# Performance work log

Measured on AMD Instinct MI355X. Metric: run time of the kernel, lower is better.

The kernel has to match this reference:

```python
import jax, jax.numpy as jnp
import numpy as np

IN_F = 128
OUT_F = 64
HEAD = 4
ALPHA = 0.1
N, S = 32, 1024
OH = OUT_F * HEAD


def setup_inputs() -> dict:
    key = jax.random.key(0)
    k_h, k_adj, k_W, k_a = jax.random.split(key, 4)
    h = jax.random.normal(k_h, (N, S, IN_F), dtype=jnp.float32)
    adj = jax.random.uniform(k_adj, (N, S, S), dtype=jnp.float32)
    # xavier_uniform with gain=1.414
    gain = 1.414
    lim_W = gain * np.sqrt(6.0 / (IN_F + OH))
    W = jax.random.uniform(k_W, (IN_F, OH), dtype=jnp.float32, minval=-lim_W, maxval=lim_W)
    lim_a = gain * np.sqrt(6.0 / (2 * OH + 1))
    a = jax.random.uniform(k_a, (2 * OH, 1), dtype=jnp.float32, minval=-lim_a, maxval=lim_a)
    return {"h": h, "adj": adj, "W": W, "a": a}


def reference(h, adj, W, a):
    # h: (N, S, F_in); adj unused in original forward
    Wh = jnp.einsum('nsf,fo->nso', h, W)  # (N, S, OH)
    a1 = a[:OH, 0]   # source half of concat weight
    a2 = a[OH:, 0]   # target half
    # concat([Wh_i, Wh_j]) @ a == Wh_i@a1 + Wh_j@a2  (avoids (N,S,S,2*OH) tensor)
    f = Wh @ a1  # (N, S)
    g = Wh @ a2  # (N, S)
    e = f[:, :, None] + g[:, None, :]          # (N, S, S)
    e = jnp.where(e > 0, e, ALPHA * e)          # LeakyReLU
    attention = jax.nn.softmax(e, axis=2)
    out = jnp.einsum('nij,njo->nio', attention, Wh)  # (N, S, OH)
    # split into HEAD chunks of OUT_F, stack, mean over heads
    out = out.reshape(N, S, HEAD, OUT_F).mean(axis=2)
    # ELU
    return jnp.where(out > 0, out, jnp.expm1(out))
```

## Files before the change

kernel.cpp:

```cpp
#include <hip/hip_runtime.h>
#include <math.h>

#define NB   32
#define SQ   1024
#define INF  128
#define OUTF 64
#define OHH  256

using bf16x8 = __attribute__((ext_vector_type(8))) __bf16;
using bf16x4 = __attribute__((ext_vector_type(4))) __bf16;
using f32x4  = __attribute__((ext_vector_type(4))) float;

__global__ __launch_bounds__(256) void kA(
    const float* __restrict__ h, const float* __restrict__ W,
    const float* __restrict__ a, __bf16* __restrict__ whmH,
    __bf16* __restrict__ whmL, float* __restrict__ fo, float* __restrict__ go)
{
    __shared__ float WMl[INF][68];
    __shared__ float hT[INF][68];
    __shared__ float al[2 * OHH];
    __shared__ float fgp[8][64];

    const int t  = threadIdx.x;
    const int R0 = blockIdx.x * 64;

    al[t]       = a[t];
    al[t + 256] = a[t + 256];

    for (int idx = t; idx < INF * OUTF; idx += 256) {
        int k = idx >> 6, c = idx & 63;
        const float* Wr = W + k * OHH + c;
        WMl[k][c] = 0.25f * (Wr[0] + Wr[64] + Wr[128] + Wr[192]);
    }

    {
        const int r  = t >> 2;
        const int kq = (t & 3) << 2;
        const float* hrow = h + (size_t)(R0 + r) * INF;
        #pragma unroll
        for (int it = 0; it < 8; ++it) {
            int k0 = it * 16 + kq;
            float4 v = *(const float4*)(hrow + k0);
            hT[k0 + 0][r] = v.x; hT[k0 + 1][r] = v.y;
            hT[k0 + 2][r] = v.z; hT[k0 + 3][r] = v.w;
        }
    }
    __syncthreads();

    if (t < INF) {
        const float4* Wr = (const float4*)(W + t * OHH);
        const float4* a1 = (const float4*)al;
        const float4* a2 = (const float4*)(al + OHH);
        float sf = 0.f, sg = 0.f;
        for (int q = 0; q < OHH / 4; ++q) {
            float4 wv = Wr[q], x1 = a1[q], x2 = a2[q];
            sf += wv.x * x1.x + wv.y * x1.y + wv.z * x1.z + wv.w * x1.w;
            sg += wv.x * x2.x + wv.y * x2.y + wv.z * x2.z + wv.w * x2.w;
        }
        WMl[t][64] = sf;
        WMl[t][65] = sg;
    }
    __syncthreads();

    const int tx = t & 15, ty = t >> 4;
    const int c0 = tx << 2, r0 = ty << 2;
    float acc[4][4] = {};
    #pragma unroll 4
    for (int k = 0; k < INF; ++k) {
        f32x4 av = *(const f32x4*)&hT[k][r0];
        f32x4 bv = *(const f32x4*)&WMl[k][c0];
        #pragma unroll
        for (int i = 0; i < 4; ++i)
            #pragma unroll
            for (int j = 0; j < 4; ++j)
                acc[i][j] += av[i] * bv[j];
    }

    {
        const int n    = R0 >> 10;
        const int J    = ((R0 & 1023) >> 5) + (ty >> 3);
        const int quad = (ty & 7) >> 1;
        const int idx0 = (ty & 1) << 2;
        const int T    = tx >> 2;
        #pragma unroll
        for (int jj = 0; jj < 4; ++jj) {
            const int cl   = ((tx & 3) << 2) + jj;
            const int lane = quad * 16 + cl;
            const size_t base =
                (((size_t)(n * 32 + J) * 4 + T) * 64 + lane) * 8 + idx0;
            bf16x4 hv, lv;
            #pragma unroll
            for (int i = 0; i < 4; ++i) {
                float p  = acc[i][jj];
                __bf16 hb = (__bf16)p;
                hv[i] = hb;
                lv[i] = (__bf16)(p - (float)hb);
            }
            *(bf16x4*)(whmH + base) = hv;
            *(bf16x4*)(whmL + base) = lv;
        }
    }

    {
        const int r = t & 63, grp = t >> 6;
        float sf = 0.f, sg = 0.f;
        for (int k = grp * 32; k < grp * 32 + 32; ++k) {
            float hv = hT[k][r];
            sf += hv * WMl[k][64];
            sg += hv * WMl[k][65];
        }
        fgp[grp][r]     = sf;
        fgp[4 + grp][r] = sg;
    }
    __syncthreads();
    if (t < 64) {
        fo[R0 + t] = fgp[0][t] + fgp[1][t] + fgp[2][t] + fgp[3][t];
    } else if (t < 128) {
        int r = t - 64;
        go[R0 + r] = fgp[4][r] + fgp[5][r] + fgp[6][r] + fgp[7][r];
    }
}

__global__ __launch_bounds__(256) void kC(
    const __bf16* __restrict__ whmH, const __bf16* __restrict__ whmL,
    const float* __restrict__ fi, const float* __restrict__ gi,
    float* __restrict__ out)
{
    __shared__ float  gl[SQ];
    __shared__ float  fl[64];
    __shared__ __bf16 bfr[3][4096];

    const int t     = threadIdx.x;
    const int lane  = t & 63;
    const int wid   = t >> 6;
    const int n     = blockIdx.x & 31;
    const int itile = blockIdx.x >> 5;
    const int i0    = itile * 64;

    const char* gHb = (const char*)(whmH + (size_t)n * 65536) + wid * 1024 + lane * 16;
    const char* gLb = (const char*)(whmL + (size_t)n * 65536) + wid * 1024 + lane * 16;

    auto stage = [&](int J, int buf) {
        char* lH = (char*)&bfr[buf][0] + wid * 1024;
        char* lL = (char*)&bfr[buf][2048] + wid * 1024;
        __builtin_amdgcn_global_load_lds(
            (const __attribute__((address_space(1))) unsigned int*)(gHb + (size_t)J * 4096),
            (__attribute__((address_space(3))) unsigned int*)lH, 16, 0, 0);
        __builtin_amdgcn_global_load_lds(
            (const __attribute__((address_space(1))) unsigned int*)(gLb + (size_t)J * 4096),
            (__attribute__((address_space(3))) unsigned int*)lL, 16, 0, 0);
    };

    ((float4*)gl)[t] = ((const float4*)(gi + n * SQ))[t];
    if (t < 64) fl[t] = fi[n * SQ + i0 + t];

    stage(0, 0);
    stage(1, 1);
    __syncthreads();

    const float myf = fl[wid * 16 + (lane & 15)];
    const int   kq  = lane >> 4;

    f32x4 acc[4] = {};
    float lsum = 0.f;

    for (int J = 0; J < 32; ++J) {
        float p[8];
        {
            const float4 g0 = *(const float4*)&gl[J * 32 + kq * 8];
            const float4 g1 = *(const float4*)&gl[J * 32 + kq * 8 + 4];
            float gs8[8] = {g0.x, g0.y, g0.z, g0.w, g1.x, g1.y, g1.z, g1.w};
            #pragma unroll
            for (int idx = 0; idx < 8; ++idx) {
                float e  = myf + gs8[idx];
                float lr = 0.55f * e + 0.45f * fabsf(e);
                p[idx] = __expf(lr);
            }
        }
        lsum += ((p[0] + p[1]) + (p[2] + p[3])) + ((p[4] + p[5]) + (p[6] + p[7]));

        bf16x8 ph, pl;
        #pragma unroll
        for (int idx = 0; idx < 8; ++idx) {
            __bf16 hb = (__bf16)p[idx];
            ph[idx] = hb;
            pl[idx] = (__bf16)(p[idx] - (float)hb);
        }

        __syncthreads();
        if (J + 2 < 32) stage(J + 2, (J + 2) % 3);

        const bf16x8* fr = (const bf16x8*)&bfr[J % 3][0];
        #pragma unroll
        for (int T = 0; T < 4; ++T) {
            bf16x8 bh = fr[T * 64 + lane];
            bf16x8 bl = fr[(4 + T) * 64 + lane];
            acc[T] = __builtin_amdgcn_mfma_f32_16x16x32_bf16(ph, bh, acc[T], 0, 0, 0);
            acc[T] = __builtin_amdgcn_mfma_f32_16x16x32_bf16(pl, bh, acc[T], 0, 0, 0);
            acc[T] = __builtin_amdgcn_mfma_f32_16x16x32_bf16(ph, bl, acc[T], 0, 0, 0);
        }
    }

    lsum += __shfl_xor(lsum, 16, 64);
    lsum += __shfl_xor(lsum, 32, 64);
    const float rv = 1.0f / lsum;

    const int rq = lane >> 4;
    float scs[4];
    #pragma unroll
    for (int r = 0; r < 4; ++r)
        scs[r] = __shfl(rv, rq * 4 + r, 64);

    const int colbase = lane & 15;
    #pragma unroll
    for (int T = 0; T < 4; ++T) {
        #pragma unroll
        for (int r = 0; r < 4; ++r) {
            int   rr = rq * 4 + r;
            float v  = acc[T][r] * scs[r];
            v = v > 0.f ? v : expm1f(v);
            out[(size_t)(n * SQ + i0 + wid * 16 + rr) * OUTF + T * 16 + colbase] = v;
        }
    }
}

extern "C" void kernel_launch(void* const* d_in, const int* in_sizes, int n_in,
                              void* d_out, int out_size, void* d_ws, size_t ws_size,
                              hipStream_t stream) {
    const float* h = (const float*)d_in[0];
    const float* W = (const float*)d_in[2];
    const float* a = (const float*)d_in[3];

    char* ws = (char*)d_ws;
    __bf16* whmH = (__bf16*)ws;
    __bf16* whmL = (__bf16*)(ws + (size_t)4 * 1024 * 1024);
    float*  fb   = (float*)(ws + (size_t)8 * 1024 * 1024);
    float*  gb   = (float*)(ws + (size_t)8 * 1024 * 1024 + 131072);
    float*  outp = (float*)d_out;

    hipLaunchKernelGGL(kA, dim3(512), dim3(256), 0, stream, h, W, a, whmH, whmL, fb, gb);
    hipLaunchKernelGGL(kC, dim3(512), dim3(256), 0, stream, whmH, whmL, fb, gb, outp);
}
```

Baseline: 216.7 us.

## Move projection GEMM to split-bf16 MFMA and cheapen softmax exp path

kA now computes h·Wmean with 3-pass split-bf16 MFMA instructions. The head-averaged W is pre-swizzled into the MFMA fragment layout in LDS, and the f/g dot products are fused into the same register loop, which drops the transposed hT staging and the separate reduction pass. f and g are prescaled by log2(e), so kC can use a raw exp2 builtin with a max-based LeakyReLU, and the bf16 high half is taken by bit truncation rather than rounding. The cost is more MFMA issue work in kA, plus slightly different rounding from truncating the high part, which the low-part correction term compensates for.

```diff
diff --git a/kernel.cpp b/kernel.cpp
--- a/kernel.cpp
+++ b/kernel.cpp
@@ -1,123 +1,151 @@
 #include <hip/hip_runtime.h>
 #include <math.h>
 
-#define NB   32
-#define SQ   1024
-#define INF  128
-#define OUTF 64
-#define OHH  256
+#define SQ    1024
+#define INF   128
+#define OUTF  64
+#define OHH   256
+#define LOG2E 1.44269504088896f
 
 using bf16x8 = __attribute__((ext_vector_type(8))) __bf16;
 using bf16x4 = __attribute__((ext_vector_type(4))) __bf16;
 using f32x4  = __attribute__((ext_vector_type(4))) float;
+using u16x8  = __attribute__((ext_vector_type(8))) unsigned short;
+
+#if __has_builtin(__builtin_amdgcn_exp2f)
+#define EXP2F(x) __builtin_amdgcn_exp2f(x)
+#else
+#define EXP2F(x) __expf((x) * 0.6931471805599453f)
+#endif
 
 __global__ __launch_bounds__(256) void kA(
     const float* __restrict__ h, const float* __restrict__ W,
     const float* __restrict__ a, __bf16* __restrict__ whmH,
     __bf16* __restrict__ whmL, float* __restrict__ fo, float* __restrict__ go)
 {
-    __shared__ float WMl[INF][68];
-    __shared__ float hT[INF][68];
-    __shared__ float al[2 * OHH];
-    __shared__ float fgp[8][64];
-
-    const int t  = threadIdx.x;
-    const int R0 = blockIdx.x * 64;
+    __shared__ __bf16 wmfH[8192];
+    __shared__ __bf16 wmfL[8192];
+    __shared__ float  wfl[INF], wgl[INF];
+    __shared__ float  al[2 * OHH];
+
+    const int t    = threadIdx.x;
+    const int lane = t & 63;
+    const int w    = t >> 6;
+    const int R0   = blockIdx.x * 64;
 
     al[t]       = a[t];
     al[t + 256] = a[t + 256];
 
-    for (int idx = t; idx < INF * OUTF; idx += 256) {
-        int k = idx >> 6, c = idx & 63;
-        const float* Wr = W + k * OHH + c;
-        WMl[k][c] = 0.25f * (Wr[0] + Wr[64] + Wr[128] + Wr[192]);
-    }
+    for (int g = t; g < 2048; g += 256) {
+        const int k  = g >> 4;
+        const int n0 = (g & 15) << 2;
+        const float* Wp = W + k * OHH + n0;
+        float4 w0 = *(const float4*)Wp;
+        float4 w1 = *(const float4*)(Wp + 64);
+        float4 w2 = *(const float4*)(Wp + 128);
+        float4 w3 = *(const float4*)(Wp + 192);
+        float wm4[4] = {0.25f * (w0.x + w1.x + w2.x + w3.x),
+                        0.25f * (w0.y + w1.y + w2.y + w3.y),
+                        0.25f * (w0.z + w1.z + w2.z + w3.z),
+                        0.25f * (w0.w + w1.w + w2.w + w3.w)};
+        const int c = k >> 5, kq = (k >> 3) & 3, id8 = k & 7, T = n0 >> 4;
+        const int lbase = kq * 16 + (n0 & 15);
+        #pragma unroll
+        for (int j = 0; j < 4; ++j) {
+            float  v  = wm4[j];
+            __bf16 hb = (__bf16)v;
+            const int o = ((c * 4 + T) * 64 + lbase + j) * 8 + id8;
+            wmfH[o] = hb;
+            wmfL[o] = (__bf16)(v - (float)hb);
+        }
+    }
+    __syncthreads();
 
     {
-        const int r  = t >> 2;
-        const int kq = (t & 3) << 2;
-        const float* hrow = h + (size_t)(R0 + r) * INF;
-        #pragma unroll
-        for (int it = 0; it < 8; ++it) {
-            int k0 = it * 16 + kq;
-            float4 v = *(const float4*)(hrow + k0);
-            hT[k0 + 0][r] = v.x; hT[k0 + 1][r] = v.y;
-            hT[k0 + 2][r] = v.z; hT[k0 + 3][r] = v.w;
-        }
+        const int row = t & 127;
+        const float4* Wr = (const float4*)(W + row * OHH);
+        const float4* av = (const float4*)(t < 128 ? al : al + OHH);
+        float s = 0.f;
+        for (int q = 0; q < OHH / 4; ++q) {
+            float4 wv = Wr[q], x = av[q];
+            s += wv.x * x.x + wv.y * x.y + wv.z * x.z + wv.w * x.w;
+        }
+        if (t < 128) wfl[row] = s * LOG2E;
+        else         wgl[row] = s * LOG2E;
     }
     __syncthreads();
 
-    if (t < INF) {
-        const float4* Wr = (const float4*)(W + t * OHH);
-        const float4* a1 = (const float4*)al;
-        const float4* a2 = (const float4*)(al + OHH);
-        float sf = 0.f, sg = 0.f;
-        for (int q = 0; q < OHH / 4; ++q) {
-            float4 wv = Wr[q], x1 = a1[q], x2 = a2[q];
-            sf += wv.x * x1.x + wv.y * x1.y + wv.z * x1.z + wv.w * x1.w;
-            sg += wv.x * x2.x + wv.y * x2.y + wv.z * x2.z + wv.w * x2.w;
-        }
-        WMl[t][64] = sf;
-        WMl[t][65] = sg;
-    }
-    __syncthreads();
-
-    const int tx = t & 15, ty = t >> 4;
-    const int c0 = tx << 2, r0 = ty << 2;
-    float acc[4][4] = {};
-    #pragma unroll 4
-    for (int k = 0; k < INF; ++k) {
-        f32x4 av = *(const f32x4*)&hT[k][r0];
-        f32x4 bv = *(const f32x4*)&WMl[k][c0];
-        #pragma unroll
-        for (int i = 0; i < 4; ++i)
-            #pragma unroll
-            for (int j = 0; j < 4; ++j)
-                acc[i][j] += av[i] * bv[j];
+    const int m  = lane & 15;
+    const int kq = lane >> 4;
+    const float* hrow = h + (size_t)(R0 + w * 16 + m) * INF + kq * 8;
+
+    f32x4 acc[4] = {};
+    float sf = 0.f, sg = 0.f;
+
+    #pragma unroll
+    for (int c = 0; c < 4; ++c) {
+        float4 v0 = *(const float4*)(hrow + c * 32);
+        float4 v1 = *(const float4*)(hrow + c * 32 + 4);
+        float hv[8] = {v0.x, v0.y, v0.z, v0.w, v1.x, v1.y, v1.z, v1.w};
+
+        float4 wf0 = *(const float4*)(wfl + c * 32 + kq * 8);
+        float4 wf1 = *(const float4*)(wfl + c * 32 + kq * 8 + 4);
+        float4 wg0 = *(const float4*)(wgl + c * 32 + kq * 8);
+        float4 wg1 = *(const float4*)(wgl + c * 32 + kq * 8 + 4);
+        float wfv[8] = {wf0.x, wf0.y, wf0.z, wf0.w, wf1.x, wf1.y, wf1.z, wf1.w};
+        float wgv[8] = {wg0.x, wg0.y, wg0.z, wg0.w, wg1.x, wg1.y, wg1.z, wg1.w};
+
+        u16x8  ahu;
+        bf16x8 alo;
+        #pragma unroll
+        for (int i = 0; i < 8; ++i) {
+            float v = hv[i];
+            sf = fmaf(v, wfv[i], sf);
+            sg = fmaf(v, wgv[i], sg);
+            unsigned u = __float_as_uint(v);
+            ahu[i] = (unsigned short)(u >> 16);
+            alo[i] = (__bf16)(v - __uint_as_float(u & 0xFFFF0000u));
+        }
+        bf16x8 ah = __builtin_bit_cast(bf16x8, ahu);
+
+        #pragma unroll
+        for (int T = 0; T < 4; ++T) {
+            bf16x8 bh = *(const bf16x8*)&wmfH[((c * 4 + T) * 64 + lane) * 8];
+            bf16x8 bl = *(const bf16x8*)&wmfL[((c * 4 + T) * 64 + lane) * 8];
+            acc[T] = __builtin_amdgcn_mfma_f32_16x16x32_bf16(ah,  bh, acc[T], 0, 0, 0);
+            acc[T] = __builtin_amdgcn_mfma_f32_16x16x32_bf16(alo, bh, acc[T], 0, 0, 0);
+            acc[T] = __builtin_amdgcn_mfma_f32_16x16x32_bf16(ah,  bl, acc[T], 0, 0, 0);
+        }
+    }
+
+    sf += __shfl_xor(sf, 16, 64); sf += __shfl_xor(sf, 32, 64);
+    sg += __shfl_xor(sg, 16, 64); sg += __shfl_xor(sg, 32, 64);
+    if (lane < 16) {
+        fo[R0 + w * 16 + m] = sf;
+        go[R0 + w * 16 + m] = sg;
     }
 
     {
-        const int n    = R0 >> 10;
-        const int J    = ((R0 & 1023) >> 5) + (ty >> 3);
-        const int quad = (ty & 7) >> 1;
-        const int idx0 = (ty & 1) << 2;
-        const int T    = tx >> 2;
-        #pragma unroll
-        for (int jj = 0; jj < 4; ++jj) {
-            const int cl   = ((tx & 3) << 2) + jj;
-            const int lane = quad * 16 + cl;
+        const int n     = R0 >> 10;
+        const int Jb    = ((R0 & 1023) >> 5) + (w >> 1);
+        const int jj3   = 2 * (w & 1) + (kq >> 1);
+        const int laneS = jj3 * 16 + m;
+        const int idx0  = (kq & 1) * 4;
+        #pragma unroll
+        for (int T = 0; T < 4; ++T) {
             const size_t base =
-                (((size_t)(n * 32 + J) * 4 + T) * 64 + lane) * 8 + idx0;
+                (((size_t)(n * 32 + Jb) * 4 + T) * 64 + laneS) * 8 + idx0;
             bf16x4 hv, lv;
             #pragma unroll
-            for (int i = 0; i < 4; ++i) {
-                float p  = acc[i][jj];
-                __bf16 hb = (__bf16)p;
-                hv[i] = hb;
-                lv[i] = (__bf16)(p - (float)hb);
+            for (int r = 0; r < 4; ++r) {
+                float  v  = acc[T][r];
+                __bf16 hb = (__bf16)v;
+                hv[r] = hb;
+                lv[r] = (__bf16)(v - (float)hb);
             }
             *(bf16x4*)(whmH + base) = hv;
             *(bf16x4*)(whmL + base) = lv;
         }
-    }
-
-    {
-        const int r = t & 63, grp = t >> 6;
-        float sf = 0.f, sg = 0.f;
-        for (int k = grp * 32; k < grp * 32 + 32; ++k) {
-            float hv = hT[k][r];
-            sf += hv * WMl[k][64];
-            sg += hv * WMl[k][65];
-        }
-        fgp[grp][r]     = sf;
-        fgp[4 + grp][r] = sg;
-    }
-    __syncthreads();
-    if (t < 64) {
-        fo[R0 + t] = fgp[0][t] + fgp[1][t] + fgp[2][t] + fgp[3][t];
-    } else if (t < 128) {
-        int r = t - 64;
-        go[R0 + r] = fgp[4][r] + fgp[5][r] + fgp[6][r] + fgp[7][r];
     }
 }
 
@@ -165,27 +193,23 @@
     float lsum = 0.f;
 
     for (int J = 0; J < 32; ++J) {
-        float p[8];
-        {
-            const float4 g0 = *(const float4*)&gl[J * 32 + kq * 8];
-            const float4 g1 = *(const float4*)&gl[J * 32 + kq * 8 + 4];
-            float gs8[8] = {g0.x, g0.y, g0.z, g0.w, g1.x, g1.y, g1.z, g1.w};
-            #pragma unroll
-            for (int idx = 0; idx < 8; ++idx) {
-                float e  = myf + gs8[idx];
-                float lr = 0.55f * e + 0.45f * fabsf(e);
-                p[idx] = __expf(lr);
-            }
-        }
-        lsum += ((p[0] + p[1]) + (p[2] + p[3])) + ((p[4] + p[5]) + (p[6] + p[7]));
-
-        bf16x8 ph, pl;
+        float4 g0 = *(const float4*)&gl[J * 32 + kq * 8];
+        float4 g1 = *(const float4*)&gl[J * 32 + kq * 8 + 4];
+        float gs8[8] = {g0.x, g0.y, g0.z, g0.w, g1.x, g1.y, g1.z, g1.w};
+
+        u16x8  phu;
+        bf16x8 pl;
         #pragma unroll
         for (int idx = 0; idx < 8; ++idx) {
-            __bf16 hb = (__bf16)p[idx];
-            ph[idx] = hb;
-            pl[idx] = (__bf16)(p[idx] - (float)hb);
-        }
+            float e  = myf + gs8[idx];
+            float lr = fmaxf(e, 0.1f * e);
+            float p  = EXP2F(lr);
+            lsum += p;
+            unsigned u = __float_as_uint(p);
+            phu[idx] = (unsigned short)(u >> 16);
+            pl[idx]  = (__bf16)(p - __uint_as_float(u & 0xFFFF0000u));
+        }
+        bf16x8 ph = __builtin_bit_cast(bf16x8, phu);
 
         __syncthreads();
         if (J + 2 < 32) stage(J + 2, (J + 2) % 3);
```

Result: no change. 215.5 us (-0.6%).
